# Kernel optimization log

Hardware: AMD Instinct MI355X
Metric: run time of the kernel (lower is better)

The kernel has to match this reference:

```python
import jax, jax.numpy as jnp
import numpy as np


def _mlp3(x, w0, b0, w1, b1, w2, b2):
    x = jax.nn.relu(x @ w0.T + b0)
    x = jax.nn.relu(x @ w1.T + b1)
    return x @ w2.T + b2


def setup_inputs() -> dict:
    key = jax.random.key(0)
    ks = jax.random.split(key, 32)
    B, T, C, E, H, A = 64, 256, 53, 64, 64, 128
    C2 = C * C
    s = 0.1  # weight scale for numerical stability
    inp = {
        'x': jax.random.normal(ks[0], (B, T, C), jnp.float32),
        'w_emb': s * jax.random.normal(ks[1], (E, 1), jnp.float32),
        'b_emb': s * jax.random.normal(ks[2], (E,), jnp.float32),
        'w_ih': s * jax.random.normal(ks[3], (3 * H, E), jnp.float32),
        'w_hh': s * jax.random.normal(ks[4], (3 * H, H), jnp.float32),
        'b_ih': s * jax.random.normal(ks[5], (3 * H,), jnp.float32),
        'b_hh': s * jax.random.normal(ks[6], (3 * H,), jnp.float32),
        'q_w0': s * jax.random.normal(ks[7], (A, H), jnp.float32),
        'q_b0': s * jax.random.normal(ks[8], (A,), jnp.float32),
        'q_w1': s * jax.random.normal(ks[9], (A, A), jnp.float32),
        'q_b1': s * jax.random.normal(ks[10], (A,), jnp.float32),
        'q_w2': s * jax.random.normal(ks[11], (A, A), jnp.float32),
        'q_b2': s * jax.random.normal(ks[12], (A,), jnp.float32),
        'k_w0': s * jax.random.normal(ks[13], (A, H), jnp.float32),
        'k_b0': s * jax.random.normal(ks[14], (A,), jnp.float32),
        'k_w1': s * jax.random.normal(ks[15], (A, A), jnp.float32),
        'k_b1': s * jax.random.normal(ks[16], (A,), jnp.float32),
        'k_w2': s * jax.random.normal(ks[17], (A, A), jnp.float32),
        'k_b2': s * jax.random.normal(ks[18], (A,), jnp.float32),
        'gate_bias': jax.random.normal(ks[19], (C, C), jnp.float32),
        'pred_w': s * jax.random.normal(ks[20], (1, H), jnp.float32),
        'pred_b': s * jax.random.normal(ks[21], (1,), jnp.float32),
        'clf_w0': 0.02 * jax.random.normal(ks[22], (C2 // 2, C2), jnp.float32),
        'clf_b0': s * jax.random.normal(ks[23], (C2 // 2,), jnp.float32),
        'clf_w1': 0.02 * jax.random.normal(ks[24], (C2 // 4, C2 // 2), jnp.float32),
        'clf_b1': s * jax.random.normal(ks[25], (C2 // 4,), jnp.float32),
        'clf_w2': 0.02 * jax.random.normal(ks[26], (2, C2 // 4), jnp.float32),
        'clf_b2': s * jax.random.normal(ks[27], (2,), jnp.float32),
    }
    return inp


def reference(x, w_emb, b_emb, w_ih, w_hh, b_ih, b_hh,
              q_w0, q_b0, q_w1, q_b1, q_w2, q_b2,
              k_w0, k_b0, k_w1, k_b1, k_w2, k_b2,
              gate_bias, pred_w, pred_b,
              clf_w0, clf_b0, clf_w1, clf_b1, clf_w2, clf_b2):
    B, T, C = x.shape
    H = w_hh.shape[1]
    # single_embed Linear(1, E): embedded[b,t,c,e] = x[b,t,c]*w[e] + b[e]
    embedded = x[..., None] * w_emb[:, 0] + b_emb          # (B,T,C,E)
    emb_t = jnp.transpose(embedded, (1, 0, 2, 3))           # (T,B,C,E)
    h0 = jnp.zeros((B, C, H), x.dtype)

    def step(h, e_t):
        # GRU cell over B*C independent sequences (vectorized as (B,C,*))
        gi = e_t @ w_ih.T + b_ih                            # (B,C,3H)
        gh = h @ w_hh.T + b_hh
        ir, iz, inn = jnp.split(gi, 3, axis=-1)
        hr, hz, hn = jnp.split(gh, 3, axis=-1)
        r = jax.nn.sigmoid(ir + hr)
        z = jax.nn.sigmoid(iz + hz)
        n = jnp.tanh(inn + r * hn)
        h_gru = (1.0 - z) * n + z * h                       # (B,C,H)
        # gated self-attention mixing across components
        q = _mlp3(h_gru, q_w0, q_b0, q_w1, q_b1, q_w2, q_b2)
        k = _mlp3(h_gru, k_w0, k_b0, k_w1, k_b1, k_w2, k_b2)
        transfer = jnp.einsum('bch,bdh->bcd', q, k)         # (B,C,C)
        norms = jnp.sqrt(jnp.sum(transfer * transfer, axis=(1, 2), keepdims=True))
        transfer = transfer / norms                         # Frobenius matrix-norm divide
        gate = jax.nn.sigmoid(jnp.abs(transfer) + gate_bias)
        transfer = transfer * gate
        h_new = jnp.einsum('bcd,bdh->bch', transfer, h_gru)
        return h_new, (h_new, transfer)

    _, (hs, mix) = jax.lax.scan(step, h0, emb_t)
    hs = jnp.transpose(hs, (1, 0, 2, 3))                    # (B,T,C,H)
    mix = jnp.transpose(mix, (1, 0, 2, 3))                  # (B,T,C,C)

    hidden = hs[:, :-1]                                     # (B,T-1,C,H)
    predicted = (hidden @ pred_w.T + pred_b)[..., 0]        # (B,T-1,C)

    clf_in = mix.reshape(B, T, -1)                          # (B,T,C^2)
    mean_FNC = jnp.mean(clf_in, axis=1).reshape(B, C, C)
    z1 = jax.nn.relu(clf_in @ clf_w0.T + clf_b0)            # dropout is identity (eval)
    z2 = jax.nn.relu(z1 @ clf_w1.T + clf_b1)
    logits = jnp.mean(z2 @ clf_w2.T + clf_b2, axis=1)       # (B,2)
    return (logits, mean_FNC, mix, predicted, x[:, 1:, :])
```

## Files before the change

kernel.cpp:

```cpp
#include <hip/hip_runtime.h>
#include <hip/hip_fp16.h>

typedef _Float16 f16;
typedef f16 f16x4 __attribute__((ext_vector_type(4)));
typedef f16 f16x8 __attribute__((ext_vector_type(8)));
typedef float f32x4 __attribute__((ext_vector_type(4)));
typedef float f32x4u __attribute__((ext_vector_type(4), aligned(4)));

#define DEVINL __device__ __forceinline__
#define MFMA16(a, b, c) __builtin_amdgcn_mfma_f32_16x16x32_f16(a, b, c, 0, 0, 0)

DEVINL float sigmoidf_(float v) { return 1.f / (1.f + __expf(-v)); }


__global__ __launch_bounds__(512)
void scan_kernel(const float* __restrict__ x,
                 const float* __restrict__ w_emb,
                 const float* __restrict__ b_emb,
                 const float* __restrict__ w_ih,
                 const float* __restrict__ w_hh,
                 const float* __restrict__ b_ih,
                 const float* __restrict__ b_hh,
                 const float* __restrict__ qw0, const float* __restrict__ qb0,
                 const float* __restrict__ qw1, const float* __restrict__ qb1,
                 const float* __restrict__ qw2, const float* __restrict__ qb2,
                 const float* __restrict__ kw0, const float* __restrict__ kb0,
                 const float* __restrict__ kw1, const float* __restrict__ kb1,
                 const float* __restrict__ kw2, const float* __restrict__ kb2,
                 const float* __restrict__ gate_bias,
                 const float* __restrict__ pred_w,
                 const float* __restrict__ pred_b,
                 float* __restrict__ out_meanF,
                 float* __restrict__ out_mix,
                 float* __restrict__ out_pred,
                 float* __restrict__ out_xcopy)
{
    __shared__ __align__(16) unsigned char smem[64900];
    float* hh  = (float*)smem;
    f16*   hK  = (f16*)(smem + 15232);
    f16*   hC  = (f16*)(smem + 23424);
    f16*   qk0 = (f16*)(smem + 31616);
    f16*   qk1 = (f16*)(smem + 48000);
    f16*   gh  = (f16*)(smem + 31616);
    f16*   trK = (f16*)(smem + 31616);
    float* xc  = (float*)(smem + 64384);
    float* pw  = (float*)(smem + 64608);
    float* red = (float*)(smem + 64864);

    const int b    = blockIdx.x;
    const int tid  = threadIdx.x;
    const int wv   = tid >> 6;
    const int lane = tid & 63;
    const int quad = lane >> 4;
    const int l15  = lane & 15;
    const int colg = (wv << 3) + (lane >> 3);
    const int rsub = lane & 7;

#define FRAG(buf, kt, nt) ((buf) + ((((kt) * 4 + (nt)) * 64 + lane) * 8))

    for (int i = tid; i < 56 * 68; i += 512) hh[i] = 0.f;
    for (int i = tid; i < 4096; i += 512) { hK[i] = (f16)0.f; hC[i] = (f16)0.f; }
    if (tid < 56) xc[tid] = 0.f;
    if (tid < 64) pw[tid] = pred_w[tid];

    float a_r = 0.f, a_z = 0.f, a_n = 0.f, s_r = 0.f, s_z = 0.f, s_n = 0.f;
    for (int e = 0; e < 64; e++) {
        float we = w_emb[e], be = b_emb[e];
        float w0 = w_ih[colg * 64 + e];
        float w1 = w_ih[(64 + colg) * 64 + e];
        float w2 = w_ih[(128 + colg) * 64 + e];
        a_r += w0 * we; s_r += w0 * be;
        a_z += w1 * we; s_z += w1 * be;
        a_n += w2 * we; s_n += w2 * be;
    }
    const float c_r = s_r + b_ih[colg] + b_hh[colg];
    const float c_z = s_z + b_ih[64 + colg] + b_hh[64 + colg];
    const float c_n = s_n + b_ih[128 + colg];
    const float bhn = b_hh[128 + colg];
    const float pb  = pred_b[0];

    auto ldfrag = [&](const float* W, int K, int mt, int kt) -> f16x8 {
        const float* p = W + (size_t)(mt * 16 + l15) * K + kt * 32 + quad * 8;
        float4 u0 = *(const float4*)p;
        float4 u1 = *(const float4*)(p + 4);
        f16x8 a;
        a[0] = (f16)u0.x; a[1] = (f16)u0.y; a[2] = (f16)u0.z; a[3] = (f16)u0.w;
        a[4] = (f16)u1.x; a[5] = (f16)u1.y; a[6] = (f16)u1.z; a[7] = (f16)u1.w;
        return a;
    };

    const int mtLo = (6 * wv) >> 2, mtHi = (6 * wv + 5) >> 2;
    f16x8 wg0k0 = ldfrag(w_hh, 64, mtLo, 0), wg0k1 = ldfrag(w_hh, 64, mtLo, 1);
    f16x8 wg1k0 = ldfrag(w_hh, 64, mtHi, 0), wg1k1 = ldfrag(w_hh, 64, mtHi, 1);

    f16x8 wq0f[2], wk0f[2], wq1f[4], wq2f[4], wk1f[4], wk2f[4];
#pragma unroll
    for (int kt = 0; kt < 2; kt++) {
        wq0f[kt] = ldfrag(qw0, 64, wv, kt);
        wk0f[kt] = ldfrag(kw0, 64, wv, kt);
    }
#pragma unroll
    for (int kt = 0; kt < 4; kt++) {
        wq1f[kt] = ldfrag(qw1, 128, wv, kt);
        wq2f[kt] = ldfrag(qw2, 128, wv, kt);
        wk1f[kt] = ldfrag(kw1, 128, wv, kt);
        wk2f[kt] = ldfrag(kw2, 128, wv, kt);
    }

    const int f0 = wv * 16 + quad * 4;
    f32x4 bq0v, bq1v, bq2v, bk0v, bk1v, bk2v;
#pragma unroll
    for (int r = 0; r < 4; r++) {
        bq0v[r] = qb0[f0 + r]; bq1v[r] = qb1[f0 + r]; bq2v[r] = qb2[f0 + r];
        bk0v[r] = kb0[f0 + r]; bk1v[r] = kb1[f0 + r]; bk2v[r] = kb2[f0 + r];
    }

    const int tmt = wv & 3, tnt0 = (wv >> 2) * 2;
    float gbv[8], mf[8];
#pragma unroll
    for (int i = 0; i < 2; i++)
#pragma unroll
        for (int r = 0; r < 4; r++) {
            int c = tmt * 16 + quad * 4 + r, d = (tnt0 + i) * 16 + l15;
            gbv[i * 4 + r] = (c < 53 && d < 53) ? gate_bias[c * 53 + d] : 0.f;
            mf[i * 4 + r] = 0.f;
        }

    auto cwrite = [&](f16* dst, int ct, const f32x4 acc, const f32x4 bv, bool rel) {
        const int kts  = wv >> 1;
        const int sub  = (2 * wv + (quad >> 1)) & 3;
        const int base = ((kts * 4 + ct) * 64 + (l15 + 16 * sub)) * 8 + (quad & 1) * 4;
        f16x4 p;
#pragma unroll
        for (int r = 0; r < 4; r++) {
            float v = acc[r] + bv[r];
            if (rel) v = fmaxf(v, 0.f);
            p[r] = (f16)v;
        }
        *(f16x4*)(dst + base) = p;
    };

    __syncthreads();

    f16x8 bf[4][4];

#define PRELOAD(SRC) do { \
    _Pragma("unroll") for (int ct = 0; ct < 4; ct++) \
        _Pragma("unroll") for (int kt = 0; kt < 4; kt++) \
            bf[ct][kt] = *(const f16x8*)FRAG(SRC, kt, ct); } while (0)

#define MLP4(WF, DST, BV, REL) do { \
    f32x4 a0 = {0.f,0.f,0.f,0.f}, a1 = {0.f,0.f,0.f,0.f}; \
    f32x4 a2 = {0.f,0.f,0.f,0.f}, a3 = {0.f,0.f,0.f,0.f}; \
    _Pragma("unroll") for (int kt = 0; kt < 4; kt++) { \
        a0 = MFMA16(WF[kt], bf[0][kt], a0); \
        a1 = MFMA16(WF[kt], bf[1][kt], a1); \
        a2 = MFMA16(WF[kt], bf[2][kt], a2); \
        a3 = MFMA16(WF[kt], bf[3][kt], a3); } \
    cwrite(DST, 0, a0, BV, REL); cwrite(DST, 1, a1, BV, REL); \
    cwrite(DST, 2, a2, BV, REL); cwrite(DST, 3, a3, BV, REL); } while (0)

    for (int t = 0; t < 256; t++) {
        if (tid < 53) {
            float xv = x[(b * 256 + t) * 53 + tid];
            xc[tid] = xv;
            if (t >= 1) out_xcopy[(b * 255 + (t - 1)) * 53 + tid] = xv;
        }
        {
#pragma unroll
            for (int i = 0; i < 6; i++) {
                int tau = 6 * wv + i, mt = tau >> 2, ct = tau & 3;
                bool hi = (mt != mtLo);
                f32x4 acc = {0.f, 0.f, 0.f, 0.f};
                acc = MFMA16(hi ? wg1k0 : wg0k0, *(const f16x8*)FRAG(hK, 0, ct), acc);
                acc = MFMA16(hi ? wg1k1 : wg0k1, *(const f16x8*)FRAG(hK, 1, ct), acc);
                int gbase = (mt * 16 + quad * 4) * 68 + ct * 16 + l15;
#pragma unroll
                for (int r = 0; r < 4; r++) gh[gbase + r * 68] = (f16)acc[r];
            }
        }
        __syncthreads();
        {
#pragma unroll
            for (int r = 0; r < 7; r++) {
                int c = rsub + 8 * r;
                float hr = (float)gh[colg * 68 + c];
                float hz = (float)gh[(64 + colg) * 68 + c];
                float hn = (float)gh[(128 + colg) * 68 + c];
                float xv = xc[c];
                float hp = hh[c * 68 + colg];
                float rr = sigmoidf_(xv * a_r + c_r + hr);
                float zz = sigmoidf_(xv * a_z + c_z + hz);
                float nn = tanhf(xv * a_n + c_n + rr * (hn + bhn));
                float hg = (1.f - zz) * nn + zz * hp;
                hh[c * 68 + colg] = hg;
                f16 h6 = (f16)hg;
                hK[(((colg >> 5) * 4 + (c >> 4)) * 64 + (c & 15) + 16 * ((colg >> 3) & 3)) * 8 + (colg & 7)] = h6;
                hC[(((c >> 5) * 4 + (colg >> 4)) * 64 + (colg & 15) + 16 * ((c >> 3) & 3)) * 8 + (c & 7)] = h6;
            }
        }
        __syncthreads();
        {
            f32x4 a0 = {0.f,0.f,0.f,0.f}, a1 = {0.f,0.f,0.f,0.f};
            f32x4 a2 = {0.f,0.f,0.f,0.f}, a3 = {0.f,0.f,0.f,0.f};
#pragma unroll
            for (int kt = 0; kt < 2; kt++) {
                a0 = MFMA16(wq0f[kt], *(const f16x8*)FRAG(hK, kt, 0), a0);
                a1 = MFMA16(wq0f[kt], *(const f16x8*)FRAG(hK, kt, 1), a1);
                a2 = MFMA16(wq0f[kt], *(const f16x8*)FRAG(hK, kt, 2), a2);
                a3 = MFMA16(wq0f[kt], *(const f16x8*)FRAG(hK, kt, 3), a3);
            }
            cwrite(qk0, 0, a0, bq0v, true); cwrite(qk0, 1, a1, bq0v, true);
            cwrite(qk0, 2, a2, bq0v, true); cwrite(qk0, 3, a3, bq0v, true);
            f32x4 k0 = {0.f,0.f,0.f,0.f}, k1 = {0.f,0.f,0.f,0.f};
            f32x4 k2 = {0.f,0.f,0.f,0.f}, k3 = {0.f,0.f,0.f,0.f};
#pragma unroll
            for (int kt = 0; kt < 2; kt++) {
                k0 = MFMA16(wk0f[kt], *(const f16x8*)FRAG(hK, kt, 0), k0);
                k1 = MFMA16(wk0f[kt], *(const f16x8*)FRAG(hK, kt, 1), k1);
                k2 = MFMA16(wk0f[kt], *(const f16x8*)FRAG(hK, kt, 2), k2);
                k3 = MFMA16(wk0f[kt], *(const f16x8*)FRAG(hK, kt, 3), k3);
            }
            cwrite(qk1, 0, k0, bk0v, true); cwrite(qk1, 1, k1, bk0v, true);
            cwrite(qk1, 2, k2, bk0v, true); cwrite(qk1, 3, k3, bk0v, true);
        }
        __syncthreads();
        PRELOAD(qk0);
        __syncthreads();
        MLP4(wq1f, qk0, bq1v, true);
        PRELOAD(qk1);
        __syncthreads();
        MLP4(wk1f, qk1, bk1v, true);
        PRELOAD(qk0);
        __syncthreads();
        MLP4(wq2f, qk0, bq2v, false);
        PRELOAD(qk1);
        __syncthreads();
        MLP4(wk2f, qk1, bk2v, false);
        __syncthreads();
        f32x4 tacc0 = {0.f,0.f,0.f,0.f}, tacc1 = {0.f,0.f,0.f,0.f};
        {
            f16x8 qa[4];
#pragma unroll
            for (int kt = 0; kt < 4; kt++) qa[kt] = *(const f16x8*)FRAG(qk0, kt, tmt);
#pragma unroll
            for (int kt = 0; kt < 4; kt++) {
                tacc0 = MFMA16(qa[kt], *(const f16x8*)FRAG(qk1, kt, tnt0), tacc0);
                tacc1 = MFMA16(qa[kt], *(const f16x8*)FRAG(qk1, kt, tnt0 + 1), tacc1);
            }
            float ssq = 0.f;
#pragma unroll
            for (int r = 0; r < 4; r++) {
                int c = tmt * 16 + quad * 4 + r;
                if (c < 53) {
                    if (tnt0 * 16 + l15 < 53)       ssq += tacc0[r] * tacc0[r];
                    if ((tnt0 + 1) * 16 + l15 < 53) ssq += tacc1[r] * tacc1[r];
                }
            }
#pragma unroll
            for (int off = 32; off > 0; off >>= 1) ssq += __shfl_down(ssq, off);
            if (lane == 0) red[wv] = ssq;
        }
        __syncthreads();
        if (tid == 0) {
            float s2 = 0.f;
            for (int w8 = 0; w8 < 8; w8++) s2 += red[w8];
            red[8] = rsqrtf(s2);
        }
        __syncthreads();
        {
            const float inv = red[8];
            const int mixbase = (b * 256 + t) * 2809;
#pragma unroll
            for (int i = 0; i < 2; i++)
#pragma unroll
                for (int r = 0; r < 4; r++) {
                    int c = tmt * 16 + quad * 4 + r;
                    int d = (tnt0 + i) * 16 + l15;
                    float v = (i == 0 ? tacc0[r] : tacc1[r]) * inv;
                    float g = sigmoidf_(fabsf(v) + gbv[i * 4 + r]);
                    v *= g;
                    bool ok = (c < 53) & (d < 53);
                    v = ok ? v : 0.f;
                    if (ok) out_mix[mixbase + c * 53 + d] = v;
                    mf[i * 4 + r] += v;
                    trK[(((d >> 5) * 4 + (c >> 4)) * 64 + (c & 15) + 16 * ((d >> 3) & 3)) * 8 + (d & 7)] = (f16)v;
                }
        }
        __syncthreads();
        {
            f32x4 h0 = {0.f,0.f,0.f,0.f}, h1 = {0.f,0.f,0.f,0.f};
            f16x8 ta0 = *(const f16x8*)FRAG(trK, 0, tmt);
            f16x8 ta1 = *(const f16x8*)FRAG(trK, 1, tmt);
            h0 = MFMA16(ta0, *(const f16x8*)FRAG(hC, 0, tnt0), h0);
            h0 = MFMA16(ta1, *(const f16x8*)FRAG(hC, 1, tnt0), h0);
            h1 = MFMA16(ta0, *(const f16x8*)FRAG(hC, 0, tnt0 + 1), h1);
            h1 = MFMA16(ta1, *(const f16x8*)FRAG(hC, 1, tnt0 + 1), h1);
#pragma unroll
            for (int i = 0; i < 2; i++)
#pragma unroll
                for (int r = 0; r < 4; r++) {
                    int c = tmt * 16 + quad * 4 + r;
                    int e = (tnt0 + i) * 16 + l15;
                    float v = (i == 0 ? h0[r] : h1[r]);
                    if (c < 56) hh[c * 68 + e] = v;
                    hK[(((e >> 5) * 4 + (c >> 4)) * 64 + (c & 15) + 16 * ((e >> 3) & 3)) * 8 + (e & 7)] = (f16)v;
                }
        }
        __syncthreads();
        if (t < 255 && tid < 53) {
            const float* hrow = hh + tid * 68;
            float s = pb;
#pragma unroll 4
            for (int e4 = 0; e4 < 16; e4++) {
                float4 hv = *(const float4*)(hrow + e4 * 4);
                float4 wv4 = *(const float4*)(pw + e4 * 4);
                s += hv.x * wv4.x + hv.y * wv4.y + hv.z * wv4.z + hv.w * wv4.w;
            }
            out_pred[(b * 255 + t) * 53 + tid] = s;
        }
    }

#pragma unroll
    for (int i = 0; i < 2; i++)
#pragma unroll
        for (int r = 0; r < 4; r++) {
            int c = tmt * 16 + quad * 4 + r;
            int d = (tnt0 + i) * 16 + l15;
            if (c < 53 && d < 53)
                out_meanF[b * 2809 + c * 53 + d] = mf[i * 4 + r] * (1.f / 256.f);
        }
#undef FRAG
#undef PRELOAD
#undef MLP4
}


DEVINL void cvt16(const float* p, f16x8& lo, f16x8& hi) {
    f32x4u u0 = *(const f32x4u*)p;
    f32x4u u1 = *(const f32x4u*)(p + 4);
    f32x4u u2 = *(const f32x4u*)(p + 8);
    f32x4u u3 = *(const f32x4u*)(p + 12);
    lo[0] = (f16)u0.x; lo[1] = (f16)u0.y; lo[2] = (f16)u0.z; lo[3] = (f16)u0.w;
    lo[4] = (f16)u1.x; lo[5] = (f16)u1.y; lo[6] = (f16)u1.z; lo[7] = (f16)u1.w;
    hi[0] = (f16)u2.x; hi[1] = (f16)u2.y; hi[2] = (f16)u2.z; hi[3] = (f16)u2.w;
    hi[4] = (f16)u3.x; hi[5] = (f16)u3.y; hi[6] = (f16)u3.z; hi[7] = (f16)u3.w;
}

template<bool AHALF, bool COLSUM>
__global__ __launch_bounds__(256)
void clf_mfma(const void* __restrict__ Ap,
              const float* __restrict__ W,
              const float* __restrict__ bias,
              __half* __restrict__ z_out,
              float* __restrict__ colsum_out,
              int N, int K, int lda, int Kpad, int ldz)
{
    __shared__ __align__(16) f16 As[4096];
    __shared__ __align__(16) f16 Bs[4096];

    const int tid  = threadIdx.x;
    const int wv   = tid >> 6;
    const int lane = tid & 63;
    const int quad = lane >> 4;
    const int l15  = lane & 15;
    const int wm   = wv & 1;
    const int wn   = wv >> 1;
    const int m0   = blockIdx.x * 128;
    const int n0   = blockIdx.y * 128;

    const int srow = tid >> 1;
    const int skh  = (tid & 1) * 16;
    const int sdst = ((srow >> 4) * 64 + (skh >> 3) * 16 + (srow & 15)) * 8;

    f32x4 acc[4][4];
#pragma unroll
    for (int i = 0; i < 4; i++)
#pragma unroll
        for (int j = 0; j < 4; j++)
            acc[i][j] = (f32x4){0.f, 0.f, 0.f, 0.f};

    for (int k0 = 0; k0 < Kpad; k0 += 32) {
        {
            f16x8 lo, hi;
            if constexpr (AHALF) {
                const f16* p = (const f16*)Ap + (size_t)(m0 + srow) * lda + k0 + skh;
                lo = *(const f16x8*)p;
                hi = *(const f16x8*)(p + 8);
            } else {
                const float* p = (const float*)Ap + (size_t)(m0 + srow) * lda + k0 + skh;
                if (k0 + 32 <= K) {
                    cvt16(p, lo, hi);
                } else {
                    int kr = K - (k0 + skh);
#pragma unroll
                    for (int j = 0; j < 8; j++) lo[j] = (f16)((j < kr) ? p[j] : 0.f);
#pragma unroll
                    for (int j = 0; j < 8; j++) hi[j] = (f16)((j + 8 < kr) ? p[j + 8] : 0.f);
                }
            }
            *(f16x8*)(As + sdst)       = lo;
            *(f16x8*)(As + sdst + 128) = hi;
        }
        {
            f16x8 lo, hi;
#pragma unroll
            for (int j = 0; j < 8; j++) { lo[j] = (f16)0.f; hi[j] = (f16)0.f; }
            const int nrow = n0 + srow;
            if (nrow < N) {
                const float* p = W + (size_t)nrow * K + k0 + skh;
                if (k0 + 32 <= K) {
                    cvt16(p, lo, hi);
                } else {
                    int kr = K - (k0 + skh);
#pragma unroll
                    for (int j = 0; j < 8; j++) lo[j] = (f16)((j < kr) ? p[j] : 0.f);
#pragma unroll
                    for (int j = 0; j < 8; j++) hi[j] = (f16)((j + 8 < kr) ? p[j + 8] : 0.f);
                }
            }
            *(f16x8*)(Bs + sdst)       = lo;
            *(f16x8*)(Bs + sdst + 128) = hi;
        }
        __syncthreads();
        {
            f16x8 afr[4], bfr[4];
#pragma unroll
            for (int i = 0; i < 4; i++)
                afr[i] = *(const f16x8*)(As + ((wm * 4 + i) * 64 + lane) * 8);
#pragma unroll
            for (int i = 0; i < 4; i++)
                bfr[i] = *(const f16x8*)(Bs + ((wn * 4 + i) * 64 + lane) * 8);
#pragma unroll
            for (int mi = 0; mi < 4; mi++)
#pragma unroll
                for (int ni = 0; ni < 4; ni++)
                    acc[mi][ni] = MFMA16(afr[mi], bfr[ni], acc[mi][ni]);
        }
        __syncthreads();
    }

    if constexpr (!COLSUM) {
#pragma unroll
        for (int ni = 0; ni < 4; ni++) {
            int n = n0 + wn * 64 + ni * 16 + l15;
            float bj = (n < N) ? bias[n] : 0.f;
#pragma unroll
            for (int mi = 0; mi < 4; mi++) {
                int m = m0 + wm * 64 + mi * 16 + quad * 4;
#pragma unroll
                for (int r = 0; r < 4; r++) {
                    float v = (n < N) ? fmaxf(acc[mi][ni][r] + bj, 0.f) : 0.f;
                    z_out[(size_t)(m + r) * ldz + n] = __float2half(v);
                }
            }
        }
    } else {
        const int batch = m0 >> 8;
#pragma unroll
        for (int ni = 0; ni < 4; ni++) {
            int n = n0 + wn * 64 + ni * 16 + l15;
            float bj = (n < N) ? bias[n] : 0.f;
            float s = 0.f;
#pragma unroll
            for (int mi = 0; mi < 4; mi++)
#pragma unroll
                for (int r = 0; r < 4; r++)
                    s += fmaxf(acc[mi][ni][r] + bj, 0.f);
            s += __shfl_down(s, 32);
            s += __shfl_down(s, 16);
            if (quad == 0 && n < N)
                atomicAdd(&colsum_out[batch * 704 + n], s);
        }
    }
}

__global__ __launch_bounds__(128)
void logits_kernel(const float* __restrict__ zsum,
                   const float* __restrict__ w2,
                   const float* __restrict__ b2,
                   float* __restrict__ out)
{
    int tid = threadIdx.x;
    int bb = tid >> 1, o = tid & 1;
    const float* zs = zsum + bb * 704;
    const float* wrow = w2 + o * 702;
    float s = 0.f;
    for (int j = 0; j < 702; j++) s += zs[j] * wrow[j];
    out[bb * 2 + o] = s * (1.f / 256.f) + b2[o];
}

extern "C" void kernel_launch(void* const* d_in, const int* in_sizes, int n_in,
                              void* d_out, int out_size, void* d_ws, size_t ws_size,
                              hipStream_t stream)
{
    const float* x      = (const float*)d_in[0];
    const float* w_emb  = (const float*)d_in[1];
    const float* b_emb  = (const float*)d_in[2];
    const float* w_ih   = (const float*)d_in[3];
    const float* w_hh   = (const float*)d_in[4];
    const float* b_ih   = (const float*)d_in[5];
    const float* b_hh   = (const float*)d_in[6];
    const float* qw0 = (const float*)d_in[7];
    const float* qb0 = (const float*)d_in[8];
    const float* qw1 = (const float*)d_in[9];
    const float* qb1 = (const float*)d_in[10];
    const float* qw2 = (const float*)d_in[11];
    const float* qb2 = (const float*)d_in[12];
    const float* kw0 = (const float*)d_in[13];
    const float* kb0 = (const float*)d_in[14];
    const float* kw1 = (const float*)d_in[15];
    const float* kb1 = (const float*)d_in[16];
    const float* kw2 = (const float*)d_in[17];
    const float* kb2 = (const float*)d_in[18];
    const float* gate_bias = (const float*)d_in[19];
    const float* pred_w = (const float*)d_in[20];
    const float* pred_b = (const float*)d_in[21];
    const float* cw0 = (const float*)d_in[22];
    const float* cb0 = (const float*)d_in[23];
    const float* cw1 = (const float*)d_in[24];
    const float* cb1 = (const float*)d_in[25];
    const float* cw2 = (const float*)d_in[26];
    const float* cb2 = (const float*)d_in[27];

    float* out_logits = (float*)d_out;
    float* out_meanF  = (float*)d_out + 128;
    float* out_mix    = (float*)d_out + 128 + 179776;
    float* out_pred   = out_mix + 46022656;
    float* out_xcopy  = out_pred + 864960;

    float*  zsum = (float*)d_ws;
    __half* z1   = (__half*)((char*)d_ws + (1 << 18));

    hipMemsetAsync(zsum, 0, 64 * 704 * sizeof(float), stream);

    scan_kernel<<<64, 512, 0, stream>>>(
        x, w_emb, b_emb, w_ih, w_hh, b_ih, b_hh,
        qw0, qb0, qw1, qb1, qw2, qb2,
        kw0, kb0, kw1, kb1, kw2, kb2,
        gate_bias, pred_w, pred_b,
        out_meanF, out_mix, out_pred, out_xcopy);

    clf_mfma<false, false><<<dim3(128, 11), 256, 0, stream>>>(
        out_mix, cw0, cb0, z1, nullptr, 1404, 2809, 2809, 2816, 1408);

    clf_mfma<true, true><<<dim3(128, 6), 256, 0, stream>>>(
        z1, cw1, cb1, nullptr, zsum, 702, 1404, 1408, 1408, 0);

    logits_kernel<<<1, 128, 0, stream>>>(zsum, cw2, cb2, out_logits);
}
```

Before: 3.091 ms.

## Double-buffer MLP activations to cut per-step barriers and prefetch inputs

Adds two extra LDS buffers (qk2/qk3) so the MLP layers read from one buffer and write to another. This removes the register preload plus barrier pairs and cuts the per-step barriers in the MLP chain from five to two. The norm reduction is now done redundantly by every thread instead of tid 0 plus an extra barrier. The x load for the next step is prefetched, and the out_mix global stores are moved after the barrier. tanhf is replaced with an exp-based formula, and shared memory grows to about 97KB of dynamic LDS.

```diff
diff --git a/kernel.cpp b/kernel.cpp
--- a/kernel.cpp
+++ b/kernel.cpp
@@ -35,17 +35,19 @@
                  float* __restrict__ out_pred,
                  float* __restrict__ out_xcopy)
 {
-    __shared__ __align__(16) unsigned char smem[64900];
+    extern __shared__ __align__(16) unsigned char smem[];
     float* hh  = (float*)smem;
     f16*   hK  = (f16*)(smem + 15232);
     f16*   hC  = (f16*)(smem + 23424);
     f16*   qk0 = (f16*)(smem + 31616);
     f16*   qk1 = (f16*)(smem + 48000);
+    f16*   qk2 = (f16*)(smem + 64384);
+    f16*   qk3 = (f16*)(smem + 80768);
     f16*   gh  = (f16*)(smem + 31616);
     f16*   trK = (f16*)(smem + 31616);
-    float* xc  = (float*)(smem + 64384);
-    float* pw  = (float*)(smem + 64608);
-    float* red = (float*)(smem + 64864);
+    float* xc  = (float*)(smem + 97152);
+    float* pw  = (float*)(smem + 97376);
+    float* red = (float*)(smem + 97632);
 
     const int b    = blockIdx.x;
     const int tid  = threadIdx.x;
@@ -142,30 +144,22 @@
 
     __syncthreads();
 
-    f16x8 bf[4][4];
-
-#define PRELOAD(SRC) do { \
-    _Pragma("unroll") for (int ct = 0; ct < 4; ct++) \
-        _Pragma("unroll") for (int kt = 0; kt < 4; kt++) \
-            bf[ct][kt] = *(const f16x8*)FRAG(SRC, kt, ct); } while (0)
-
-#define MLP4(WF, DST, BV, REL) do { \
+#define MLP4X(WF, SRC, DST, BV, REL) do { \
     f32x4 a0 = {0.f,0.f,0.f,0.f}, a1 = {0.f,0.f,0.f,0.f}; \
     f32x4 a2 = {0.f,0.f,0.f,0.f}, a3 = {0.f,0.f,0.f,0.f}; \
     _Pragma("unroll") for (int kt = 0; kt < 4; kt++) { \
-        a0 = MFMA16(WF[kt], bf[0][kt], a0); \
-        a1 = MFMA16(WF[kt], bf[1][kt], a1); \
-        a2 = MFMA16(WF[kt], bf[2][kt], a2); \
-        a3 = MFMA16(WF[kt], bf[3][kt], a3); } \
+        a0 = MFMA16(WF[kt], *(const f16x8*)FRAG(SRC, kt, 0), a0); \
+        a1 = MFMA16(WF[kt], *(const f16x8*)FRAG(SRC, kt, 1), a1); \
+        a2 = MFMA16(WF[kt], *(const f16x8*)FRAG(SRC, kt, 2), a2); \
+        a3 = MFMA16(WF[kt], *(const f16x8*)FRAG(SRC, kt, 3), a3); } \
     cwrite(DST, 0, a0, BV, REL); cwrite(DST, 1, a1, BV, REL); \
     cwrite(DST, 2, a2, BV, REL); cwrite(DST, 3, a3, BV, REL); } while (0)
 
+    float xv = 0.f;
+    if (tid < 53) xv = x[(size_t)b * 256 * 53 + tid];
+
     for (int t = 0; t < 256; t++) {
-        if (tid < 53) {
-            float xv = x[(b * 256 + t) * 53 + tid];
-            xc[tid] = xv;
-            if (t >= 1) out_xcopy[(b * 255 + (t - 1)) * 53 + tid] = xv;
-        }
+        if (tid < 53) xc[tid] = xv;
         {
 #pragma unroll
             for (int i = 0; i < 6; i++) {
@@ -187,11 +181,12 @@
                 float hr = (float)gh[colg * 68 + c];
                 float hz = (float)gh[(64 + colg) * 68 + c];
                 float hn = (float)gh[(128 + colg) * 68 + c];
-                float xv = xc[c];
+                float xcv = xc[c];
                 float hp = hh[c * 68 + colg];
-                float rr = sigmoidf_(xv * a_r + c_r + hr);
-                float zz = sigmoidf_(xv * a_z + c_z + hz);
-                float nn = tanhf(xv * a_n + c_n + rr * (hn + bhn));
+                float rr = sigmoidf_(xcv * a_r + c_r + hr);
+                float zz = sigmoidf_(xcv * a_z + c_z + hz);
+                float e2 = __expf(2.f * (xcv * a_n + c_n + rr * (hn + bhn)));
+                float nn = 1.f - 2.f / (e2 + 1.f);
                 float hg = (1.f - zz) * nn + zz * hp;
                 hh[c * 68 + colg] = hg;
                 f16 h6 = (f16)hg;
@@ -201,6 +196,10 @@
         }
         __syncthreads();
         {
+            if (tid < 53) {
+                if (t >= 1) out_xcopy[(b * 255 + (t - 1)) * 53 + tid] = xv;
+                if (t < 255) xv = x[((size_t)b * 256 + t + 1) * 53 + tid];
+            }
             f32x4 a0 = {0.f,0.f,0.f,0.f}, a1 = {0.f,0.f,0.f,0.f};
             f32x4 a2 = {0.f,0.f,0.f,0.f}, a3 = {0.f,0.f,0.f,0.f};
 #pragma unroll
@@ -225,18 +224,11 @@
             cwrite(qk1, 2, k2, bk0v, true); cwrite(qk1, 3, k3, bk0v, true);
         }
         __syncthreads();
-        PRELOAD(qk0);
-        __syncthreads();
-        MLP4(wq1f, qk0, bq1v, true);
-        PRELOAD(qk1);
-        __syncthreads();
-        MLP4(wk1f, qk1, bk1v, true);
-        PRELOAD(qk0);
-        __syncthreads();
-        MLP4(wq2f, qk0, bq2v, false);
-        PRELOAD(qk1);
-        __syncthreads();
-        MLP4(wk2f, qk1, bk2v, false);
+        MLP4X(wq1f, qk0, qk2, bq1v, true);
+        MLP4X(wk1f, qk1, qk3, bk1v, true);
+        __syncthreads();
+        MLP4X(wq2f, qk2, qk0, bq2v, false);
+        MLP4X(wk2f, qk3, qk1, bk2v, false);
         __syncthreads();
         f32x4 tacc0 = {0.f,0.f,0.f,0.f}, tacc1 = {0.f,0.f,0.f,0.f};
         {
@@ -262,15 +254,12 @@
             if (lane == 0) red[wv] = ssq;
         }
         __syncthreads();
-        if (tid == 0) {
+        float ov[8];
+        {
             float s2 = 0.f;
+#pragma unroll
             for (int w8 = 0; w8 < 8; w8++) s2 += red[w8];
-            red[8] = rsqrtf(s2);
-        }
-        __syncthreads();
-        {
-            const float inv = red[8];
-            const int mixbase = (b * 256 + t) * 2809;
+            const float inv = rsqrtf(s2);
 #pragma unroll
             for (int i = 0; i < 2; i++)
 #pragma unroll
@@ -282,12 +271,23 @@
                     v *= g;
                     bool ok = (c < 53) & (d < 53);
                     v = ok ? v : 0.f;
-                    if (ok) out_mix[mixbase + c * 53 + d] = v;
+                    ov[i * 4 + r] = v;
                     mf[i * 4 + r] += v;
                     trK[(((d >> 5) * 4 + (c >> 4)) * 64 + (c & 15) + 16 * ((d >> 3) & 3)) * 8 + (d & 7)] = (f16)v;
                 }
         }
         __syncthreads();
+        {
+            const int mixbase = (b * 256 + t) * 2809;
+#pragma unroll
+            for (int i = 0; i < 2; i++)
+#pragma unroll
+                for (int r = 0; r < 4; r++) {
+                    int c = tmt * 16 + quad * 4 + r;
+                    int d = (tnt0 + i) * 16 + l15;
+                    if ((c < 53) & (d < 53)) out_mix[mixbase + c * 53 + d] = ov[i * 4 + r];
+                }
+        }
         {
             f32x4 h0 = {0.f,0.f,0.f,0.f}, h1 = {0.f,0.f,0.f,0.f};
             f16x8 ta0 = *(const f16x8*)FRAG(trK, 0, tmt);
@@ -331,10 +331,8 @@
                 out_meanF[b * 2809 + c * 53 + d] = mf[i * 4 + r] * (1.f / 256.f);
         }
 #undef FRAG
-#undef PRELOAD
-#undef MLP4
+#undef MLP4X
 }
-
 
 DEVINL void cvt16(const float* p, f16x8& lo, f16x8& hi) {
     f32x4u u0 = *(const f32x4u*)p;
@@ -532,9 +530,16 @@
     float*  zsum = (float*)d_ws;
     __half* z1   = (__half*)((char*)d_ws + (1 << 18));
 
+    static int s_attr_done = 0;
+    if (!s_attr_done) {
+        hipFuncSetAttribute((const void*)scan_kernel,
+                            hipFuncAttributeMaxDynamicSharedMemorySize, 98304);
+        s_attr_done = 1;
+    }
+
     hipMemsetAsync(zsum, 0, 64 * 704 * sizeof(float), stream);
 
-    scan_kernel<<<64, 512, 0, stream>>>(
+    scan_kernel<<<64, 512, 97680, stream>>>(
         x, w_emb, b_emb, w_ih, w_hh, b_ih, b_hh,
         qw0, qb0, qw1, qb1, qw2, qb2,
         kw0, kb0, kw1, kb1, kw2, kb2,
```

Result: slower. 3.217 ms (+4.1%).

## Pack two batch sequences per 1024-thread block and trim scan-loop syncs

Applied to the files above, without the earlier changes.

The scan kernel now runs two independent batch elements per block (1024 threads, 32 blocks) with separate dynamic shared-memory halves. The x load is software-prefetched one step ahead, the norm reduction is done redundantly by every thread to drop one barrier, out_mix stores are moved after the barrier, and tanh is replaced with an exp-based formula. The aim is to cut per-step latency in the serial recurrence. The cost is that block-wide barriers now couple two sequences, the register budget per thread may shrink under 1024-thread launch bounds, and the 130 KB shared allocation leaves fewer spare resources per CU.

```diff
diff --git a/kernel.cpp b/kernel.cpp
--- a/kernel.cpp
+++ b/kernel.cpp
@@ -13,7 +13,7 @@
 DEVINL float sigmoidf_(float v) { return 1.f / (1.f + __expf(-v)); }
 
 
-__global__ __launch_bounds__(512)
+__global__ __launch_bounds__(1024)
 void scan_kernel(const float* __restrict__ x,
                  const float* __restrict__ w_emb,
                  const float* __restrict__ b_emb,
@@ -35,33 +35,38 @@
                  float* __restrict__ out_pred,
                  float* __restrict__ out_xcopy)
 {
-    __shared__ __align__(16) unsigned char smem[64900];
-    float* hh  = (float*)smem;
-    f16*   hK  = (f16*)(smem + 15232);
-    f16*   hC  = (f16*)(smem + 23424);
-    f16*   qk0 = (f16*)(smem + 31616);
-    f16*   qk1 = (f16*)(smem + 48000);
-    f16*   gh  = (f16*)(smem + 31616);
-    f16*   trK = (f16*)(smem + 31616);
-    float* xc  = (float*)(smem + 64384);
-    float* pw  = (float*)(smem + 64608);
-    float* red = (float*)(smem + 64864);
-
-    const int b    = blockIdx.x;
+    extern __shared__ __align__(16) unsigned char smem[];
+
     const int tid  = threadIdx.x;
-    const int wv   = tid >> 6;
+    const int p    = tid >> 9;
+    const int htid = tid & 511;
+    const int wv   = htid >> 6;
     const int lane = tid & 63;
     const int quad = lane >> 4;
     const int l15  = lane & 15;
     const int colg = (wv << 3) + (lane >> 3);
     const int rsub = lane & 7;
 
+    unsigned char* base = smem + p * 65024;
+    float* hh  = (float*)base;
+    f16*   hK  = (f16*)(base + 15232);
+    f16*   hC  = (f16*)(base + 23424);
+    f16*   qk0 = (f16*)(base + 31616);
+    f16*   qk1 = (f16*)(base + 48000);
+    f16*   gh  = (f16*)(base + 31616);
+    f16*   trK = (f16*)(base + 31616);
+    float* xc  = (float*)(base + 64384);
+    float* pw  = (float*)(base + 64608);
+    float* red = (float*)(base + 64864);
+
+    const int b = (int)blockIdx.x * 2 + p;
+
 #define FRAG(buf, kt, nt) ((buf) + ((((kt) * 4 + (nt)) * 64 + lane) * 8))
 
-    for (int i = tid; i < 56 * 68; i += 512) hh[i] = 0.f;
-    for (int i = tid; i < 4096; i += 512) { hK[i] = (f16)0.f; hC[i] = (f16)0.f; }
-    if (tid < 56) xc[tid] = 0.f;
-    if (tid < 64) pw[tid] = pred_w[tid];
+    for (int i = htid; i < 56 * 68; i += 512) hh[i] = 0.f;
+    for (int i = htid; i < 4096; i += 512) { hK[i] = (f16)0.f; hC[i] = (f16)0.f; }
+    if (htid < 56) xc[htid] = 0.f;
+    if (htid < 64) pw[htid] = pred_w[htid];
 
     float a_r = 0.f, a_z = 0.f, a_n = 0.f, s_r = 0.f, s_z = 0.f, s_n = 0.f;
     for (int e = 0; e < 64; e++) {
@@ -80,9 +85,9 @@
     const float pb  = pred_b[0];
 
     auto ldfrag = [&](const float* W, int K, int mt, int kt) -> f16x8 {
-        const float* p = W + (size_t)(mt * 16 + l15) * K + kt * 32 + quad * 8;
-        float4 u0 = *(const float4*)p;
-        float4 u1 = *(const float4*)(p + 4);
+        const float* ptr = W + (size_t)(mt * 16 + l15) * K + kt * 32 + quad * 8;
+        float4 u0 = *(const float4*)ptr;
+        float4 u1 = *(const float4*)(ptr + 4);
         f16x8 a;
         a[0] = (f16)u0.x; a[1] = (f16)u0.y; a[2] = (f16)u0.z; a[3] = (f16)u0.w;
         a[4] = (f16)u1.x; a[5] = (f16)u1.y; a[6] = (f16)u1.z; a[7] = (f16)u1.w;
@@ -129,15 +134,15 @@
     auto cwrite = [&](f16* dst, int ct, const f32x4 acc, const f32x4 bv, bool rel) {
         const int kts  = wv >> 1;
         const int sub  = (2 * wv + (quad >> 1)) & 3;
-        const int base = ((kts * 4 + ct) * 64 + (l15 + 16 * sub)) * 8 + (quad & 1) * 4;
-        f16x4 p;
+        const int bofs = ((kts * 4 + ct) * 64 + (l15 + 16 * sub)) * 8 + (quad & 1) * 4;
+        f16x4 pk;
 #pragma unroll
         for (int r = 0; r < 4; r++) {
             float v = acc[r] + bv[r];
             if (rel) v = fmaxf(v, 0.f);
-            p[r] = (f16)v;
-        }
-        *(f16x4*)(dst + base) = p;
+            pk[r] = (f16)v;
+        }
+        *(f16x4*)(dst + bofs) = pk;
     };
 
     __syncthreads();
@@ -160,12 +165,11 @@
     cwrite(DST, 0, a0, BV, REL); cwrite(DST, 1, a1, BV, REL); \
     cwrite(DST, 2, a2, BV, REL); cwrite(DST, 3, a3, BV, REL); } while (0)
 
+    float xv = 0.f;
+    if (htid < 53) xv = x[(size_t)b * 256 * 53 + htid];
+
     for (int t = 0; t < 256; t++) {
-        if (tid < 53) {
-            float xv = x[(b * 256 + t) * 53 + tid];
-            xc[tid] = xv;
-            if (t >= 1) out_xcopy[(b * 255 + (t - 1)) * 53 + tid] = xv;
-        }
+        if (htid < 53) xc[htid] = xv;
         {
 #pragma unroll
             for (int i = 0; i < 6; i++) {
@@ -187,11 +191,12 @@
                 float hr = (float)gh[colg * 68 + c];
                 float hz = (float)gh[(64 + colg) * 68 + c];
                 float hn = (float)gh[(128 + colg) * 68 + c];
-                float xv = xc[c];
+                float xcv = xc[c];
                 float hp = hh[c * 68 + colg];
-                float rr = sigmoidf_(xv * a_r + c_r + hr);
-                float zz = sigmoidf_(xv * a_z + c_z + hz);
-                float nn = tanhf(xv * a_n + c_n + rr * (hn + bhn));
+                float rr = sigmoidf_(xcv * a_r + c_r + hr);
+                float zz = sigmoidf_(xcv * a_z + c_z + hz);
+                float e2 = __expf(2.f * (xcv * a_n + c_n + rr * (hn + bhn)));
+                float nn = 1.f - 2.f / (e2 + 1.f);
                 float hg = (1.f - zz) * nn + zz * hp;
                 hh[c * 68 + colg] = hg;
                 f16 h6 = (f16)hg;
@@ -201,6 +206,10 @@
         }
         __syncthreads();
         {
+            if (htid < 53) {
+                if (t >= 1) out_xcopy[((size_t)b * 255 + (t - 1)) * 53 + htid] = xv;
+                if (t < 255) xv = x[((size_t)b * 256 + t + 1) * 53 + htid];
+            }
             f32x4 a0 = {0.f,0.f,0.f,0.f}, a1 = {0.f,0.f,0.f,0.f};
             f32x4 a2 = {0.f,0.f,0.f,0.f}, a3 = {0.f,0.f,0.f,0.f};
 #pragma unroll
@@ -262,15 +271,12 @@
             if (lane == 0) red[wv] = ssq;
         }
         __syncthreads();
-        if (tid == 0) {
+        float ov[8];
+        {
             float s2 = 0.f;
+#pragma unroll
             for (int w8 = 0; w8 < 8; w8++) s2 += red[w8];
-            red[8] = rsqrtf(s2);
-        }
-        __syncthreads();
-        {
-            const float inv = red[8];
-            const int mixbase = (b * 256 + t) * 2809;
+            const float inv = rsqrtf(s2);
 #pragma unroll
             for (int i = 0; i < 2; i++)
 #pragma unroll
@@ -282,12 +288,23 @@
                     v *= g;
                     bool ok = (c < 53) & (d < 53);
                     v = ok ? v : 0.f;
-                    if (ok) out_mix[mixbase + c * 53 + d] = v;
+                    ov[i * 4 + r] = v;
                     mf[i * 4 + r] += v;
                     trK[(((d >> 5) * 4 + (c >> 4)) * 64 + (c & 15) + 16 * ((d >> 3) & 3)) * 8 + (d & 7)] = (f16)v;
                 }
         }
         __syncthreads();
+        {
+            const size_t mixbase = ((size_t)b * 256 + t) * 2809;
+#pragma unroll
+            for (int i = 0; i < 2; i++)
+#pragma unroll
+                for (int r = 0; r < 4; r++) {
+                    int c = tmt * 16 + quad * 4 + r;
+                    int d = (tnt0 + i) * 16 + l15;
+                    if ((c < 53) & (d < 53)) out_mix[mixbase + c * 53 + d] = ov[i * 4 + r];
+                }
+        }
         {
             f32x4 h0 = {0.f,0.f,0.f,0.f}, h1 = {0.f,0.f,0.f,0.f};
             f16x8 ta0 = *(const f16x8*)FRAG(trK, 0, tmt);
@@ -308,8 +325,8 @@
                 }
         }
         __syncthreads();
-        if (t < 255 && tid < 53) {
-            const float* hrow = hh + tid * 68;
+        if (t < 255 && htid < 53) {
+            const float* hrow = hh + htid * 68;
             float s = pb;
 #pragma unroll 4
             for (int e4 = 0; e4 < 16; e4++) {
@@ -317,7 +334,7 @@
                 float4 wv4 = *(const float4*)(pw + e4 * 4);
                 s += hv.x * wv4.x + hv.y * wv4.y + hv.z * wv4.z + hv.w * wv4.w;
             }
-            out_pred[(b * 255 + t) * 53 + tid] = s;
+            out_pred[((size_t)b * 255 + t) * 53 + htid] = s;
         }
     }
 
@@ -328,13 +345,12 @@
             int c = tmt * 16 + quad * 4 + r;
             int d = (tnt0 + i) * 16 + l15;
             if (c < 53 && d < 53)
-                out_meanF[b * 2809 + c * 53 + d] = mf[i * 4 + r] * (1.f / 256.f);
+                out_meanF[(size_t)b * 2809 + c * 53 + d] = mf[i * 4 + r] * (1.f / 256.f);
         }
 #undef FRAG
 #undef PRELOAD
 #undef MLP4
 }
-
 
 DEVINL void cvt16(const float* p, f16x8& lo, f16x8& hi) {
     f32x4u u0 = *(const f32x4u*)p;
@@ -532,9 +548,12 @@
     float*  zsum = (float*)d_ws;
     __half* z1   = (__half*)((char*)d_ws + (1 << 18));
 
+    hipFuncSetAttribute((const void*)scan_kernel,
+                        hipFuncAttributeMaxDynamicSharedMemorySize, 130048);
+
     hipMemsetAsync(zsum, 0, 64 * 704 * sizeof(float), stream);
 
-    scan_kernel<<<64, 512, 0, stream>>>(
+    scan_kernel<<<32, 1024, 130048, stream>>>(
         x, w_emb, b_emb, w_ih, w_hh, b_ih, b_hh,
         qw0, qb0, qw1, qb1, qw2, qb2,
         kw0, kb0, kw1, kb1, kw2, kb2,
```

Result: slower. 7.440 ms (+140.7%).

## Use LDS-only barriers, prefetch x, drop reduction barrier in scan kernel

Applied to the files above, without the earlier changes.

Replaces __syncthreads in the sequential scan loop with an s_waitcnt lgkmcnt(0)+s_barrier that does not wait for outstanding global memory ops, so global stores (mix, xcopy, pred) can overlap with later steps. Prefetches the next timestep's x value a step ahead. Removes a barrier by having every thread sum the 8 per-wave partials itself instead of thread 0 broadcasting. Also moves the mix global stores after the barrier and swaps tanhf for an exp-based formula. Correctness relies on the hand-written barrier covering only LDS hazards.

```diff
diff --git a/kernel.cpp b/kernel.cpp
--- a/kernel.cpp
+++ b/kernel.cpp
@@ -9,6 +9,8 @@
 
 #define DEVINL __device__ __forceinline__
 #define MFMA16(a, b, c) __builtin_amdgcn_mfma_f32_16x16x32_f16(a, b, c, 0, 0, 0)
+
+#define BARRIER_LDS() asm volatile("s_waitcnt lgkmcnt(0)\n\ts_barrier" ::: "memory")
 
 DEVINL float sigmoidf_(float v) { return 1.f / (1.f + __expf(-v)); }
 
@@ -130,14 +132,14 @@
         const int kts  = wv >> 1;
         const int sub  = (2 * wv + (quad >> 1)) & 3;
         const int base = ((kts * 4 + ct) * 64 + (l15 + 16 * sub)) * 8 + (quad & 1) * 4;
-        f16x4 p;
+        f16x4 pk;
 #pragma unroll
         for (int r = 0; r < 4; r++) {
             float v = acc[r] + bv[r];
             if (rel) v = fmaxf(v, 0.f);
-            p[r] = (f16)v;
-        }
-        *(f16x4*)(dst + base) = p;
+            pk[r] = (f16)v;
+        }
+        *(f16x4*)(dst + base) = pk;
     };
 
     __syncthreads();
@@ -160,12 +162,11 @@
     cwrite(DST, 0, a0, BV, REL); cwrite(DST, 1, a1, BV, REL); \
     cwrite(DST, 2, a2, BV, REL); cwrite(DST, 3, a3, BV, REL); } while (0)
 
+    float xv = 0.f;
+    if (tid < 53) xv = x[(size_t)b * 256 * 53 + tid];
+
     for (int t = 0; t < 256; t++) {
-        if (tid < 53) {
-            float xv = x[(b * 256 + t) * 53 + tid];
-            xc[tid] = xv;
-            if (t >= 1) out_xcopy[(b * 255 + (t - 1)) * 53 + tid] = xv;
-        }
+        if (tid < 53) xc[tid] = xv;
         {
 #pragma unroll
             for (int i = 0; i < 6; i++) {
@@ -179,7 +180,7 @@
                 for (int r = 0; r < 4; r++) gh[gbase + r * 68] = (f16)acc[r];
             }
         }
-        __syncthreads();
+        BARRIER_LDS();
         {
 #pragma unroll
             for (int r = 0; r < 7; r++) {
@@ -187,11 +188,12 @@
                 float hr = (float)gh[colg * 68 + c];
                 float hz = (float)gh[(64 + colg) * 68 + c];
                 float hn = (float)gh[(128 + colg) * 68 + c];
-                float xv = xc[c];
+                float xcv = xc[c];
                 float hp = hh[c * 68 + colg];
-                float rr = sigmoidf_(xv * a_r + c_r + hr);
-                float zz = sigmoidf_(xv * a_z + c_z + hz);
-                float nn = tanhf(xv * a_n + c_n + rr * (hn + bhn));
+                float rr = sigmoidf_(xcv * a_r + c_r + hr);
+                float zz = sigmoidf_(xcv * a_z + c_z + hz);
+                float e2 = __expf(2.f * (xcv * a_n + c_n + rr * (hn + bhn)));
+                float nn = 1.f - 2.f / (e2 + 1.f);
                 float hg = (1.f - zz) * nn + zz * hp;
                 hh[c * 68 + colg] = hg;
                 f16 h6 = (f16)hg;
@@ -199,8 +201,12 @@
                 hC[(((c >> 5) * 4 + (colg >> 4)) * 64 + (colg & 15) + 16 * ((c >> 3) & 3)) * 8 + (c & 7)] = h6;
             }
         }
-        __syncthreads();
-        {
+        BARRIER_LDS();
+        {
+            if (tid < 53) {
+                if (t >= 1) out_xcopy[((size_t)b * 255 + (t - 1)) * 53 + tid] = xv;
+                if (t < 255) xv = x[((size_t)b * 256 + t + 1) * 53 + tid];
+            }
             f32x4 a0 = {0.f,0.f,0.f,0.f}, a1 = {0.f,0.f,0.f,0.f};
             f32x4 a2 = {0.f,0.f,0.f,0.f}, a3 = {0.f,0.f,0.f,0.f};
 #pragma unroll
@@ -224,20 +230,20 @@
             cwrite(qk1, 0, k0, bk0v, true); cwrite(qk1, 1, k1, bk0v, true);
             cwrite(qk1, 2, k2, bk0v, true); cwrite(qk1, 3, k3, bk0v, true);
         }
-        __syncthreads();
+        BARRIER_LDS();
         PRELOAD(qk0);
-        __syncthreads();
+        BARRIER_LDS();
         MLP4(wq1f, qk0, bq1v, true);
         PRELOAD(qk1);
-        __syncthreads();
+        BARRIER_LDS();
         MLP4(wk1f, qk1, bk1v, true);
         PRELOAD(qk0);
-        __syncthreads();
+        BARRIER_LDS();
         MLP4(wq2f, qk0, bq2v, false);
         PRELOAD(qk1);
-        __syncthreads();
+        BARRIER_LDS();
         MLP4(wk2f, qk1, bk2v, false);
-        __syncthreads();
+        BARRIER_LDS();
         f32x4 tacc0 = {0.f,0.f,0.f,0.f}, tacc1 = {0.f,0.f,0.f,0.f};
         {
             f16x8 qa[4];
@@ -261,16 +267,13 @@
             for (int off = 32; off > 0; off >>= 1) ssq += __shfl_down(ssq, off);
             if (lane == 0) red[wv] = ssq;
         }
-        __syncthreads();
-        if (tid == 0) {
+        BARRIER_LDS();
+        float ov[8];
+        {
             float s2 = 0.f;
+#pragma unroll
             for (int w8 = 0; w8 < 8; w8++) s2 += red[w8];
-            red[8] = rsqrtf(s2);
-        }
-        __syncthreads();
-        {
-            const float inv = red[8];
-            const int mixbase = (b * 256 + t) * 2809;
+            const float inv = rsqrtf(s2);
 #pragma unroll
             for (int i = 0; i < 2; i++)
 #pragma unroll
@@ -282,12 +285,23 @@
                     v *= g;
                     bool ok = (c < 53) & (d < 53);
                     v = ok ? v : 0.f;
-                    if (ok) out_mix[mixbase + c * 53 + d] = v;
+                    ov[i * 4 + r] = v;
                     mf[i * 4 + r] += v;
                     trK[(((d >> 5) * 4 + (c >> 4)) * 64 + (c & 15) + 16 * ((d >> 3) & 3)) * 8 + (d & 7)] = (f16)v;
                 }
         }
-        __syncthreads();
+        BARRIER_LDS();
+        {
+            const size_t mixbase = ((size_t)b * 256 + t) * 2809;
+#pragma unroll
+            for (int i = 0; i < 2; i++)
+#pragma unroll
+                for (int r = 0; r < 4; r++) {
+                    int c = tmt * 16 + quad * 4 + r;
+                    int d = (tnt0 + i) * 16 + l15;
+                    if ((c < 53) & (d < 53)) out_mix[mixbase + c * 53 + d] = ov[i * 4 + r];
+                }
+        }
         {
             f32x4 h0 = {0.f,0.f,0.f,0.f}, h1 = {0.f,0.f,0.f,0.f};
             f16x8 ta0 = *(const f16x8*)FRAG(trK, 0, tmt);
@@ -307,7 +321,7 @@
                     hK[(((e >> 5) * 4 + (c >> 4)) * 64 + (c & 15) + 16 * ((e >> 3) & 3)) * 8 + (e & 7)] = (f16)v;
                 }
         }
-        __syncthreads();
+        BARRIER_LDS();
         if (t < 255 && tid < 53) {
             const float* hrow = hh + tid * 68;
             float s = pb;
@@ -317,7 +331,7 @@
                 float4 wv4 = *(const float4*)(pw + e4 * 4);
                 s += hv.x * wv4.x + hv.y * wv4.y + hv.z * wv4.z + hv.w * wv4.w;
             }
-            out_pred[(b * 255 + t) * 53 + tid] = s;
+            out_pred[((size_t)b * 255 + t) * 53 + tid] = s;
         }
     }
 
@@ -328,13 +342,12 @@
             int c = tmt * 16 + quad * 4 + r;
             int d = (tnt0 + i) * 16 + l15;
             if (c < 53 && d < 53)
-                out_meanF[b * 2809 + c * 53 + d] = mf[i * 4 + r] * (1.f / 256.f);
+                out_meanF[(size_t)b * 2809 + c * 53 + d] = mf[i * 4 + r] * (1.f / 256.f);
         }
 #undef FRAG
 #undef PRELOAD
 #undef MLP4
 }
-
 
 DEVINL void cvt16(const float* p, f16x8& lo, f16x8& hi) {
     f32x4u u0 = *(const f32x4u*)p;
```

Measured after the change: 3.103 ms. No clear change (+0.4%).
